# Kernel tuning notes

Measured on AMD Instinct MI355X. Metric: run time of the kernel, lower is better.

## Reference

```python
import jax, jax.numpy as jnp
import numpy as np

B, N, EMBED = 4, 2048, 512
H, EXPAND = 8, 3
D1 = (EXPAND * EMBED) // H * H   # 1536
HD = D1 // H                     # 192
RPE = int(min(EMBED / 8, 32))    # 32 (overridden in __init__)
EPS = 1e-8


def _srms(x, d):
    # SimpleRMSNorm: x / (||x||_2 * d^-0.5 + eps); no learnable params
    nrm = jnp.linalg.norm(x, axis=-1, keepdims=True)
    return x / (nrm * (d ** -0.5) + EPS)


def setup_inputs() -> dict:
    key = jax.random.key(0)
    ks = iter(jax.random.split(key, 32))
    w = lambda shape, s=0.02: jax.random.normal(next(ks), shape, dtype=jnp.float32) * s
    return {
        "xyz": jax.random.normal(next(ks), (B, N, 3), dtype=jnp.float32),
        "x": jax.random.normal(next(ks), (B, N, EMBED), dtype=jnp.float32),
        "u_w": w((EMBED, D1)), "u_b": w((D1,)),
        "v_w": w((EMBED, D1)), "v_b": w((D1,)),
        "o_w": w((D1, EMBED)), "o_b": w((EMBED,)),
        "rpe_pos_w": w((1, RPE)), "rpe_pos_b": w((RPE,)),
        "rpe_lyr_w": w((3, RPE, RPE)), "rpe_lyr_b": w((3, RPE)),
        "rpe_out_w": w((RPE, H * HD)), "rpe_out_b": w((H * HD,)),
        "glu1_w": w((EMBED, D1)), "glu1_b": w((D1,)),
        "glu2_w": w((EMBED, D1)), "glu2_b": w((D1,)),
        "glu3_w": w((D1, EMBED)), "glu3_b": w((EMBED,)),
    }


def _rpe_mlp(idx, pw, pb, lw, lb, ow, ob):
    # idx: [m, 1] positions -> [H, m, HD] Toeplitz coefficients
    h = jax.nn.relu(idx @ pw + pb)
    for i in range(lw.shape[0]):  # fixed small layer count (3), non-residual
        h = jax.nn.relu(_srms(h, RPE)) @ lw[i] + lb[i]
    o = jax.nn.relu(_srms(h, RPE)) @ ow + ob  # [m, H*HD]
    return o.reshape(-1, H, HD).transpose(1, 0, 2)


def reference(xyz, x, u_w, u_b, v_w, v_b, o_w, o_b,
              rpe_pos_w, rpe_pos_b, rpe_lyr_w, rpe_lyr_b,
              rpe_out_w, rpe_out_b,
              glu1_w, glu1_b, glu2_w, glu2_b, glu3_w, glu3_b):
    b, n, _ = x.shape
    shortcut = x
    # NOTE: original builds SimpleRMSNorm(d1) but applies it to embed_dim
    # features, so the divisor uses d1^-0.5. Preserved faithfully.
    xn = _srms(x, D1)
    u = jax.nn.silu(xn @ u_w + u_b)                      # b n d1
    v = jax.nn.silu(xn @ v_w + v_b)
    v = v.reshape(b, n, H, HD).transpose(0, 2, 1, 3)     # b h n d
    # --- Tno non-causal (par_type=1, no decay, act_type='none') ---
    rpe = lambda idx: _rpe_mlp(idx, rpe_pos_w, rpe_pos_b, rpe_lyr_w,
                               rpe_lyr_b, rpe_out_w, rpe_out_b)
    zero = rpe(jnp.zeros((1, 1), dtype=x.dtype))                     # h 1 d
    pos = rpe(jnp.arange(1, n, dtype=x.dtype)[:, None])              # h n-1 d
    neg = rpe(-jnp.arange(n - 1, 0, -1, dtype=x.dtype)[:, None])     # h n-1 d
    a = jnp.concatenate([zero, pos, zero, neg], axis=1)              # h 2n d
    # Toeplitz matmul as length-2n circular convolution via FFT
    yf = jnp.fft.rfft(v, 2 * n, axis=-2)
    af = jnp.fft.rfft(a, 2 * n, axis=-2)[None]
    t = jnp.fft.irfft(yf * af, 2 * n, axis=-2)[:, :, :n, :]          # b h n d
    t = t.transpose(0, 2, 1, 3).reshape(b, n, D1)
    out = (u * t) @ o_w + o_b
    x2 = out + shortcut
    # GLU (fina_act='None', dropout=0)
    g = (jax.nn.silu(x2 @ glu1_w + glu1_b) * (x2 @ glu2_w + glu2_b)) @ glu3_w + glu3_b
    return (g, out)
```

## Files before the change

kernel.cpp:

```cpp
#include <hip/hip_runtime.h>
#include <math.h>

#define NSEQ 2048
#define NFFT 4096
#define D1C  1536
#define EMBC 512
#define BATCH 4

typedef __fp16 f16;
typedef __fp16 f16x8 __attribute__((ext_vector_type(8)));
typedef __fp16 f16x4 __attribute__((ext_vector_type(4)));
typedef float  f32x4 __attribute__((ext_vector_type(4)));
typedef unsigned int u32;

__device__ __forceinline__ float silu_f(float y) { return y / (1.f + expf(-y)); }

__global__ __launch_bounds__(256) void scale_kernel(const float* __restrict__ x,
                                                    float* __restrict__ scale) {
    int row  = blockIdx.x * 4 + (threadIdx.x >> 6);
    int lane = threadIdx.x & 63;
    const float* xr = x + (size_t)row * EMBC;
    float ss = 0.f;
#pragma unroll
    for (int k = 0; k < EMBC / 64; ++k) { float v = xr[lane + k * 64]; ss += v * v; }
#pragma unroll
    for (int off = 32; off >= 1; off >>= 1) ss += __shfl_xor(ss, off);
    if (lane == 0) scale[row] = 1.f / (sqrtf(ss) * 0.02551551815399144f + 1e-8f);
}

__global__ __launch_bounds__(256) void convert_xn_kernel(
    const float* __restrict__ x, const float* __restrict__ scale,
    f16* __restrict__ xh, f16* __restrict__ xl) {
    size_t i = ((size_t)blockIdx.x * 256 + threadIdx.x) * 4;
    float4 v = *reinterpret_cast<const float4*>(x + i);
    float s = scale[i >> 9];
    f16x4 h, l;
    const float* vv = (const float*)&v;
#pragma unroll
    for (int j = 0; j < 4; ++j) {
        float val = vv[j] * s;
        f16 hh = (f16)val;
        h[j] = hh; l[j] = (f16)(val - (float)hh);
    }
    *reinterpret_cast<f16x4*>(xh + i) = h;
    *reinterpret_cast<f16x4*>(xl + i) = l;
}

__global__ __launch_bounds__(256) void convert_x2_kernel(
    const float* __restrict__ a, const float* __restrict__ b,
    f16* __restrict__ xh, f16* __restrict__ xl) {
    size_t i = ((size_t)blockIdx.x * 256 + threadIdx.x) * 4;
    float4 va = *reinterpret_cast<const float4*>(a + i);
    float4 vb = *reinterpret_cast<const float4*>(b + i);
    const float* pa = (const float*)&va;
    const float* pb = (const float*)&vb;
    f16x4 h, l;
#pragma unroll
    for (int j = 0; j < 4; ++j) {
        float val = pa[j] + pb[j];
        f16 hh = (f16)val;
        h[j] = hh; l[j] = (f16)(val - (float)hh);
    }
    *reinterpret_cast<f16x4*>(xh + i) = h;
    *reinterpret_cast<f16x4*>(xl + i) = l;
}

__global__ __launch_bounds__(256) void wtrans_kernel(const float* __restrict__ W,
        f16* __restrict__ Th, int Kd, int Nd) {
    __shared__ float t[32][33];
    int tx = threadIdx.x & 31, ty = threadIdx.x >> 5;
    int n0 = blockIdx.x * 32, k0 = blockIdx.y * 32;
#pragma unroll
    for (int yy = ty; yy < 32; yy += 8)
        t[yy][tx] = W[(size_t)(k0 + yy) * Nd + n0 + tx];
    __syncthreads();
#pragma unroll
    for (int yy = ty; yy < 32; yy += 8) {
        float v = t[tx][yy];
        Th[(size_t)(n0 + yy) * Kd + k0 + tx] = (f16)v;
    }
}

__global__ __launch_bounds__(256) void convert_p_kernel(
    const float* __restrict__ u, const float* __restrict__ vt,
    f16* __restrict__ ph, f16* __restrict__ pl) {
    __shared__ float t[32][33];
    int b = blockIdx.z, n0 = blockIdx.x * 32, c0 = blockIdx.y * 32;
    int tx = threadIdx.x & 31, ty = threadIdx.x >> 5;
#pragma unroll
    for (int yy = ty; yy < 32; yy += 8)
        t[yy][tx] = vt[(((size_t)(b * D1C + c0 + yy)) << 11) + n0 + tx];
    __syncthreads();
#pragma unroll
    for (int yy = ty; yy < 32; yy += 8) {
        int row = b * NSEQ + n0 + yy;
        size_t idx = (size_t)row * D1C + c0 + tx;
        float val = u[idx] * t[tx][yy];
        f16 h = (f16)val;
        ph[idx] = h; pl[idx] = (f16)(val - (float)h);
    }
}

__global__ __launch_bounds__(256) void rpe_kernel(
    const float* __restrict__ pw, const float* __restrict__ pb,
    const float* __restrict__ lw, const float* __restrict__ lb,
    const float* __restrict__ ow, const float* __restrict__ ob,
    float* __restrict__ a_r) {
    __shared__ float hs[64][33];
    int tid = threadIdx.x;
    int s0  = blockIdx.x * 64;
    if (tid < 64) {
        int s = s0 + tid;
        float p = (s == 0 || s == 2048) ? 0.f : (s < 2048 ? (float)s : (float)(s - 4096));
        float h[32];
#pragma unroll
        for (int k = 0; k < 32; ++k) h[k] = fmaxf(p * pw[k] + pb[k], 0.f);
        for (int L = 0; L < 3; ++L) {
            float ss = 0.f;
#pragma unroll
            for (int k = 0; k < 32; ++k) ss += h[k] * h[k];
            float sc = 1.f / (sqrtf(ss) * 0.1767766952966369f + 1e-8f);
            float g[32];
#pragma unroll
            for (int k = 0; k < 32; ++k) g[k] = fmaxf(h[k] * sc, 0.f);
#pragma unroll
            for (int j = 0; j < 32; ++j) {
                float acc = lb[L * 32 + j];
#pragma unroll
                for (int k = 0; k < 32; ++k) acc += g[k] * lw[(L * 32 + k) * 32 + j];
                h[j] = acc;
            }
        }
        float ss = 0.f;
#pragma unroll
        for (int k = 0; k < 32; ++k) ss += h[k] * h[k];
        float sc = 1.f / (sqrtf(ss) * 0.1767766952966369f + 1e-8f);
#pragma unroll
        for (int k = 0; k < 32; ++k) hs[tid][k] = fmaxf(h[k] * sc, 0.f);
    }
    __syncthreads();
    for (int cc = 0; cc < 6; ++cc) {
        int col = tid + cc * 256;
        float wcol[32];
#pragma unroll
        for (int k = 0; k < 32; ++k) wcol[k] = ow[k * D1C + col];
        float bb = ob[col];
        float* outp = a_r + ((size_t)col << 12) + s0;
        for (int r = 0; r < 64; ++r) {
            float acc = bb;
#pragma unroll
            for (int k = 0; k < 32; ++k) acc += hs[r][k] * wcol[k];
            outp[r] = acc;
        }
    }
}

#define LIDX(e) ((e) + ((((e) >> 4)) << 1))

template <bool INV, bool HALF>
__device__ __forceinline__ void dft16(const float* xr, const float* xi,
                                      float* outr, float* outi) {
    constexpr float C1 = 0.92387953251f, S1 = 0.38268343236f, R2 = 0.70710678119f;
    constexpr float sg = INV ? 1.f : -1.f;
    float tr[16], ti[16];
#pragma unroll
    for (int n0 = 0; n0 < 4; ++n0) {
        float ar = xr[n0], ai = xi[n0];
        float br = xr[n0 + 4], bi = xi[n0 + 4];
        float j0r, j0i, j1r, j1i, j2r, j2i, j3r, j3i;
        if constexpr (HALF) {
            j0r = ar + br; j0i = ai + bi;
            j2r = ar - br; j2i = ai - bi;
            if constexpr (!INV) { j1r = ar + bi; j1i = ai - br; j3r = ar - bi; j3i = ai + br; }
            else                { j1r = ar - bi; j1i = ai + br; j3r = ar + bi; j3i = ai - br; }
        } else {
            float cr = xr[n0 + 8],  ci = xi[n0 + 8];
            float dr = xr[n0 + 12], di = xi[n0 + 12];
            float t0r = ar + cr, t0i = ai + ci;
            float t1r = ar - cr, t1i = ai - ci;
            float t2r = br + dr, t2i = bi + di;
            float t3r = br - dr, t3i = bi - di;
            j0r = t0r + t2r; j0i = t0i + t2i;
            j2r = t0r - t2r; j2i = t0i - t2i;
            if constexpr (!INV) { j1r = t1r + t3i; j1i = t1i - t3r;
                                  j3r = t1r - t3i; j3i = t1i + t3r; }
            else                { j1r = t1r - t3i; j1i = t1i + t3r;
                                  j3r = t1r + t3i; j3i = t1i - t3r; }
        }
        tr[n0] = j0r;      ti[n0] = j0i;
        tr[n0 + 4] = j1r;  ti[n0 + 4] = j1i;
        tr[n0 + 8] = j2r;  ti[n0 + 8] = j2i;
        tr[n0 + 12] = j3r; ti[n0 + 12] = j3i;
    }
#define CMK(idx, wr_, wi_) { float _r = tr[idx], _i = ti[idx]; \
        tr[idx] = _r * (wr_) - _i * (wi_); ti[idx] = _r * (wi_) + _i * (wr_); }
    CMK(5,  C1, sg * S1)  CMK(6,  R2, sg * R2)  CMK(7,  S1, sg * C1)
    CMK(9,  R2, sg * R2)
    { float _r = tr[10];
      if constexpr (!INV) { tr[10] = ti[10];  ti[10] = -_r; }
      else                { tr[10] = -ti[10]; ti[10] = _r;  } }
    CMK(11, -R2, sg * R2)
    CMK(13, S1, sg * C1)  CMK(14, -R2, sg * R2)  CMK(15, -C1, -sg * S1)
#undef CMK
#pragma unroll
    for (int j = 0; j < 4; ++j) {
        float ar = tr[4 * j],     ai = ti[4 * j];
        float br = tr[4 * j + 1], bi = ti[4 * j + 1];
        float cr = tr[4 * j + 2], ci = ti[4 * j + 2];
        float dr = tr[4 * j + 3], di = ti[4 * j + 3];
        float t0r = ar + cr, t0i = ai + ci;
        float t1r = ar - cr, t1i = ai - ci;
        float t2r = br + dr, t2i = bi + di;
        float t3r = br - dr, t3i = bi - di;
        outr[j]      = t0r + t2r; outi[j]      = t0i + t2i;
        outr[8 + j]  = t0r - t2r; outi[8 + j]  = t0i - t2i;
        if constexpr (!INV) {
            outr[4 + j]  = t1r + t3i; outi[4 + j]  = t1i - t3r;
            outr[12 + j] = t1r - t3i; outi[12 + j] = t1i + t3r;
        } else {
            outr[4 + j]  = t1r - t3i; outi[4 + j]  = t1i + t3r;
            outr[12 + j] = t1r + t3i; outi[12 + j] = t1i - t3r;
        }
    }
}

#define CMUL_ADV(wr, wi, sr, si) { float _n = (wr)*(sr) - (wi)*(si); \
        (wi) = (wr)*(si) + (wi)*(sr); (wr) = _n; }

__global__ __launch_bounds__(256, 4) void fft_a_kernel(const float* __restrict__ a_r,
                                                       float2* __restrict__ af) {
    __shared__ float2 buf[4608];
    int tid = threadIdx.x;
    const float* row = a_r + ((size_t)blockIdx.x << 12);
    float2* orow     = af  + ((size_t)blockIdx.x << 12);
    float xr[16], xi[16], yr[16], yi[16];
    float bsr, bsi, wr, wi;
#pragma unroll
    for (int a = 0; a < 16; ++a) { xr[a] = row[a * 256 + tid]; xi[a] = 0.f; }
    dft16<false, false>(xr, xi, yr, yi);
    __sincosf(-(float)M_PI / 2048.f * (float)tid, &bsi, &bsr);
    wr = bsr; wi = bsi;
    buf[LIDX(tid)] = make_float2(yr[0], yi[0]);
#pragma unroll
    for (int k0 = 1; k0 < 16; ++k0) {
        buf[LIDX(k0 * 256 + tid)] =
            make_float2(yr[k0] * wr - yi[k0] * wi, yr[k0] * wi + yi[k0] * wr);
        CMUL_ADV(wr, wi, bsr, bsi);
    }
    __syncthreads();
    int k0 = tid >> 4, cc = tid & 15;
    int base2 = k0 * 256 + cc;
#pragma unroll
    for (int b = 0; b < 16; ++b) {
        float2 v = buf[LIDX(base2 + b * 16)]; xr[b] = v.x; xi[b] = v.y;
    }
    dft16<false, false>(xr, xi, yr, yi);
    __sincosf(-(float)M_PI / 128.f * (float)cc, &bsi, &bsr);
    wr = bsr; wi = bsi;
    buf[LIDX(base2)] = make_float2(yr[0], yi[0]);
#pragma unroll
    for (int k1 = 1; k1 < 16; ++k1) {
        buf[LIDX(base2 + k1 * 16)] =
            make_float2(yr[k1] * wr - yi[k1] * wi, yr[k1] * wi + yi[k1] * wr);
        CMUL_ADV(wr, wi, bsr, bsi);
    }
    __syncthreads();
    const float4* pld = (const float4*)&buf[18 * tid];
#pragma unroll
    for (int h = 0; h < 8; ++h) {
        float4 q = pld[h];
        xr[2 * h] = q.x; xi[2 * h] = q.y; xr[2 * h + 1] = q.z; xi[2 * h + 1] = q.w;
    }
    dft16<false, false>(xr, xi, yr, yi);
#pragma unroll
    for (int k2 = 0; k2 < 16; ++k2)
        orow[k2 * 256 + tid] = make_float2(yr[k2], yi[k2]);
}

__global__ __launch_bounds__(256, 4) void conv_kernel(float* __restrict__ vt,
                                                      const float2* __restrict__ af) {
    __shared__ float2 buf[4608];
    int tid = threadIdx.x;
    int pr  = blockIdx.x / D1C;
    int col = blockIdx.x % D1C;
    float* v0 = vt + ((size_t)((2 * pr)     * D1C + col) << 11);
    float* v1 = vt + ((size_t)((2 * pr + 1) * D1C + col) << 11);
    const float2* arow = af + ((size_t)col << 12);
    float xr[16], xi[16], yr[16], yi[16];
    float bsr, bsi, wr, wi;

#pragma unroll
    for (int a = 0; a < 8; ++a) { xr[a] = v0[a * 256 + tid]; xi[a] = v1[a * 256 + tid]; }
    dft16<false, true>(xr, xi, yr, yi);
    __sincosf(-(float)M_PI / 2048.f * (float)tid, &bsi, &bsr);
    wr = bsr; wi = bsi;
    buf[LIDX(tid)] = make_float2(yr[0], yi[0]);
#pragma unroll
    for (int k0 = 1; k0 < 16; ++k0) {
        buf[LIDX(k0 * 256 + tid)] =
            make_float2(yr[k0] * wr - yi[k0] * wi, yr[k0] * wi + yi[k0] * wr);
        CMUL_ADV(wr, wi, bsr, bsi);
    }
    __syncthreads();
    int k0 = tid >> 4, cc = tid & 15;
    int base2 = k0 * 256 + cc;
#pragma unroll
    for (int b = 0; b < 16; ++b) {
        float2 v = buf[LIDX(base2 + b * 16)]; xr[b] = v.x; xi[b] = v.y;
    }
    dft16<false, false>(xr, xi, yr, yi);
    __sincosf(-(float)M_PI / 128.f * (float)cc, &bsi, &bsr);
    wr = bsr; wi = bsi;
    buf[LIDX(base2)] = make_float2(yr[0], yi[0]);
#pragma unroll
    for (int k1 = 1; k1 < 16; ++k1) {
        buf[LIDX(base2 + k1 * 16)] =
            make_float2(yr[k1] * wr - yi[k1] * wi, yr[k1] * wi + yi[k1] * wr);
        CMUL_ADV(wr, wi, bsr, bsi);
    }
    __syncthreads();
    const float4* pld = (const float4*)&buf[18 * tid];
#pragma unroll
    for (int h = 0; h < 8; ++h) {
        float4 q = pld[h];
        xr[2 * h] = q.x; xi[2 * h] = q.y; xr[2 * h + 1] = q.z; xi[2 * h + 1] = q.w;
    }
    dft16<false, false>(xr, xi, yr, yi);
    const float inv = 1.0f / 4096.0f;
#pragma unroll
    for (int k2 = 0; k2 < 16; ++k2) {
        float2 w = arow[k2 * 256 + tid];
        float rr = (yr[k2] * w.x - yi[k2] * w.y) * inv;
        float ii = (yr[k2] * w.y + yi[k2] * w.x) * inv;
        xr[k2] = rr; xi[k2] = ii;
    }
    dft16<true, false>(xr, xi, yr, yi);
    __sincosf((float)M_PI / 128.f * (float)cc, &bsi, &bsr);
    wr = bsr; wi = bsi;
#pragma unroll
    for (int c = 1; c < 16; ++c) {
        float rr = yr[c] * wr - yi[c] * wi;
        yi[c] = yr[c] * wi + yi[c] * wr; yr[c] = rr;
        CMUL_ADV(wr, wi, bsr, bsi);
    }
    float4* pst = (float4*)&buf[18 * tid];
#pragma unroll
    for (int h = 0; h < 8; ++h)
        pst[h] = make_float4(yr[2 * h], yi[2 * h], yr[2 * h + 1], yi[2 * h + 1]);
    __syncthreads();
#pragma unroll
    for (int k1 = 0; k1 < 16; ++k1) {
        float2 v = buf[LIDX(base2 + k1 * 16)]; xr[k1] = v.x; xi[k1] = v.y;
    }
    dft16<true, false>(xr, xi, yr, yi);
    float swr, swi;
    __sincosf((float)M_PI / 2048.f * (float)(k0 * cc), &bsi, &bsr);
    __sincosf((float)M_PI / 128.f * (float)k0, &swi, &swr);
    wr = bsr; wi = bsi;
#pragma unroll
    for (int b = 0; b < 16; ++b) {
        buf[LIDX(base2 + b * 16)] =
            make_float2(yr[b] * wr - yi[b] * wi, yr[b] * wi + yi[b] * wr);
        CMUL_ADV(wr, wi, swr, swi);
    }
    __syncthreads();
#pragma unroll
    for (int k = 0; k < 16; ++k) {
        float2 v = buf[LIDX(k * 256 + tid)]; xr[k] = v.x; xi[k] = v.y;
    }
    dft16<true, false>(xr, xi, yr, yi);
#pragma unroll
    for (int a = 0; a < 8; ++a) {
        v0[a * 256 + tid] = yr[a];
        v1[a * 256 + tid] = yi[a];
    }
}

enum { EP_SILU_F32, EP_SILU_VT, EP_PLAIN, EP_GLU2 };

template <int BM, int K, int EPI>
__global__ __launch_bounds__(256, (BM == 128 ? 3 : 4)) void mgemm(
    const f16* __restrict__ Ah, const f16* __restrict__ Al,
    const f16* __restrict__ Bh,
    const float* __restrict__ bias, const float* __restrict__ E0,
    float* __restrict__ OutF, f16* __restrict__ OutH, f16* __restrict__ OutL,
    int Ncols) {
    constexpr int SB   = BM * 128 + 8192;
    constexpr int MREP = BM / 32;
    constexpr int LOGB = (BM == 128 ? 7 : 6);
    constexpr int CA   = BM / 64;
    __shared__ __align__(16) char smem[2 * SB];

    const int tid  = threadIdx.x;
    const int w    = tid >> 6, lane = tid & 63;
    const int wr   = w >> 1, wc = w & 1;
    const int l15  = lane & 15, kc = lane >> 4;

    const int NBY = Ncols >> 7;
    const int nwg = gridDim.x;
    int flat = blockIdx.x;
    int q8 = nwg >> 3, r8 = nwg & 7;
    int xcd = flat & 7, pos = flat >> 3;
    int wg = (xcd < r8 ? xcd * (q8 + 1) : r8 * (q8 + 1) + (xcd - r8) * q8) + pos;
    const int row0 = (wg / NBY) * BM;
    const int col0 = (wg % NBY) * 128;

    f32x4 acc[MREP][4] = {};

    auto stage = [&](int buf, int kt) {
        const int k0 = kt * 32;
        const int bb = buf * SB;
#pragma unroll
        for (int l = 0; l < CA; ++l) {
            int ci = tid + l * 256;
            int r = ci & (BM - 1), kk = ci >> LOGB;
            const f16* ga = Ah + (size_t)(row0 + r) * K + k0 + kk * 8;
            const f16* gb = Al + (size_t)(row0 + r) * K + k0 + kk * 8;
            __builtin_amdgcn_global_load_lds((const __attribute__((address_space(1))) u32*)ga,
                (__attribute__((address_space(3))) u32*)(smem + bb + ci * 16), 16, 0, 0);
            __builtin_amdgcn_global_load_lds((const __attribute__((address_space(1))) u32*)gb,
                (__attribute__((address_space(3))) u32*)(smem + bb + BM * 64 + ci * 16), 16, 0, 0);
        }
#pragma unroll
        for (int l = 0; l < 2; ++l) {
            int ci = tid + l * 256;
            int c = ci & 127, kk = ci >> 7;
            const f16* gc = Bh + (size_t)(col0 + c) * K + k0 + kk * 8;
            __builtin_amdgcn_global_load_lds((const __attribute__((address_space(1))) u32*)gc,
                (__attribute__((address_space(3))) u32*)(smem + bb + BM * 128 + ci * 16), 16, 0, 0);
        }
    };

    auto compute = [&](int buf) {
        const char* base = smem + buf * SB;
        f16x8 a_h[MREP], a_l[MREP], b_h[4];
#pragma unroll
        for (int m = 0; m < MREP; ++m) {
            int r = wr * (BM / 2) + m * 16 + l15;
            a_h[m] = *(const f16x8*)(base + (kc * BM + r) * 16);
            a_l[m] = *(const f16x8*)(base + BM * 64 + (kc * BM + r) * 16);
        }
#pragma unroll
        for (int n = 0; n < 4; ++n) {
            int c = wc * 64 + n * 16 + l15;
            b_h[n] = *(const f16x8*)(base + BM * 128 + (kc * 128 + c) * 16);
        }
#pragma unroll
        for (int m = 0; m < MREP; ++m)
#pragma unroll
            for (int n = 0; n < 4; ++n) {
                acc[m][n] = __builtin_amdgcn_mfma_f32_16x16x32_f16(a_h[m], b_h[n], acc[m][n], 0, 0, 0);
                acc[m][n] = __builtin_amdgcn_mfma_f32_16x16x32_f16(a_l[m], b_h[n], acc[m][n], 0, 0, 0);
            }
    };

    constexpr int NT = K / 32;
    stage(0, 0);
    __syncthreads();
    int cur = 0;
    for (int t = 0; t < NT; ++t) {
        if (t + 1 < NT) stage(cur ^ 1, t + 1);
        compute(cur);
        __syncthreads();
        cur ^= 1;
    }

    const int WRB = wr * (BM / 2);
    if constexpr (EPI == EP_SILU_VT) {
        float* patch = (float*)(smem + w * 5376);
#pragma unroll
        for (int m = 0; m < MREP; ++m) {
            __syncthreads();
#pragma unroll
            for (int n = 0; n < 4; ++n)
#pragma unroll
                for (int r = 0; r < 4; ++r)
                    patch[(n * 16 + l15) * 20 + kc * 4 + r] = acc[m][n][r];
            __syncthreads();
#pragma unroll
            for (int t = 0; t < 4; ++t) {
                int qi = lane + t * 64;
                int col_ = qi >> 2, rq = qi & 3;
                float4 y = *(const float4*)&patch[col_ * 20 + rq * 4];
                int col = col0 + wc * 64 + col_;
                float bb = bias[col];
                y.x = silu_f(y.x + bb); y.y = silu_f(y.y + bb);
                y.z = silu_f(y.z + bb); y.w = silu_f(y.w + bb);
                int b = row0 >> 11;
                int seq = (row0 & 2047) + WRB + m * 16 + rq * 4;
                *(float4*)&OutF[(((size_t)(b * D1C + col)) << 11) + seq] = y;
            }
        }
    } else {
        float* patch = (float*)(smem + w * 4352);
#pragma unroll
        for (int m = 0; m < MREP; ++m) {
            __syncthreads();
#pragma unroll
            for (int n = 0; n < 4; ++n)
#pragma unroll
                for (int r = 0; r < 4; ++r)
                    patch[(kc * 4 + r) * 68 + n * 16 + l15] = acc[m][n][r];
            __syncthreads();
#pragma unroll
            for (int t = 0; t < 4; ++t) {
                int qi = lane + t * 64;
                int row_ = qi >> 4, q = qi & 15;
                float4 y = *(const float4*)&patch[row_ * 68 + q * 4];
                int row = row0 + WRB + m * 16 + row_;
                int col = col0 + wc * 64 + q * 4;
                float4 bb = *(const float4*)&bias[col];
                y.x += bb.x; y.y += bb.y; y.z += bb.z; y.w += bb.w;
                size_t idx = (size_t)row * Ncols + col;
                if constexpr (EPI == EP_SILU_F32) {
                    y.x = silu_f(y.x); y.y = silu_f(y.y);
                    y.z = silu_f(y.z); y.w = silu_f(y.w);
                    *(float4*)&OutF[idx] = y;
                } else if constexpr (EPI == EP_PLAIN) {
                    *(float4*)&OutF[idx] = y;
                } else {
                    float4 e = *(const float4*)&E0[idx];
                    float z0 = e.x * y.x, z1 = e.y * y.y, z2 = e.z * y.z, z3 = e.w * y.w;
                    f16x4 h, l;
                    h[0] = (f16)z0; l[0] = (f16)(z0 - (float)h[0]);
                    h[1] = (f16)z1; l[1] = (f16)(z1 - (float)h[1]);
                    h[2] = (f16)z2; l[2] = (f16)(z2 - (float)h[2]);
                    h[3] = (f16)z3; l[3] = (f16)(z3 - (float)h[3]);
                    *(f16x4*)&OutH[idx] = h;
                    *(f16x4*)&OutL[idx] = l;
                }
            }
        }
    }
}

extern "C" void kernel_launch(void* const* d_in, const int* in_sizes, int n_in,
                              void* d_out, int out_size, void* d_ws, size_t ws_size,
                              hipStream_t stream) {
    const float* x   = (const float*)d_in[1];
    const float* u_w = (const float*)d_in[2];
    const float* u_b = (const float*)d_in[3];
    const float* v_w = (const float*)d_in[4];
    const float* v_b = (const float*)d_in[5];
    const float* o_w = (const float*)d_in[6];
    const float* o_b = (const float*)d_in[7];
    const float* rpw = (const float*)d_in[8];
    const float* rpb = (const float*)d_in[9];
    const float* rlw = (const float*)d_in[10];
    const float* rlb = (const float*)d_in[11];
    const float* row_w = (const float*)d_in[12];
    const float* rob = (const float*)d_in[13];
    const float* g1w = (const float*)d_in[14];
    const float* g1b = (const float*)d_in[15];
    const float* g2w = (const float*)d_in[16];
    const float* g2b = (const float*)d_in[17];
    const float* g3w = (const float*)d_in[18];
    const float* g3b = (const float*)d_in[19];

    char* wsb = (char*)d_ws;
    float* scale = (float*)wsb;
    char* R1 = wsb + (1 << 16);
    char* R2 = R1 + 50331648;
    char* R3 = R2 + 50331648;
    char* R4 = R3 + 50331648;
    char* R5 = R4 + 16777216;

    float2* af   = (float2*)R1;
    f16*    ph   = (f16*)R1;
    f16*    pl   = (f16*)(R1 + 25165824);
    float*  vt   = (float*)R2;
    float*  tmp1 = (float*)R2;
    float*  a_r  = (float*)R3;
    float*  u    = (float*)R3;
    f16*    zh   = (f16*)R3;
    f16*    zl   = (f16*)(R3 + 25165824);
    f16*    xnh  = (f16*)R4;
    f16*    xnl  = (f16*)(R4 + 8388608);
    f16*    x2h  = xnh;
    f16*    x2l  = xnl;

    auto wTh = [&](int i) { return (f16*)(R5 + (size_t)i * 1572864); };

    float* g_out   = (float*)d_out;
    float* out_out = g_out + (size_t)BATCH * NSEQ * EMBC;

    scale_kernel<<<2048, 256, 0, stream>>>(x, scale);
    convert_xn_kernel<<<4096, 256, 0, stream>>>(x, scale, xnh, xnl);
    wtrans_kernel<<<dim3(48, 16), 256, 0, stream>>>(u_w, wTh(0), 512, 1536);
    wtrans_kernel<<<dim3(48, 16), 256, 0, stream>>>(v_w, wTh(1), 512, 1536);
    wtrans_kernel<<<dim3(16, 48), 256, 0, stream>>>(o_w, wTh(2), 1536, 512);
    wtrans_kernel<<<dim3(48, 16), 256, 0, stream>>>(g1w, wTh(3), 512, 1536);
    wtrans_kernel<<<dim3(48, 16), 256, 0, stream>>>(g2w, wTh(4), 512, 1536);
    wtrans_kernel<<<dim3(16, 48), 256, 0, stream>>>(g3w, wTh(5), 1536, 512);
    rpe_kernel<<<64, 256, 0, stream>>>(rpw, rpb, rlw, rlb, row_w, rob, a_r);
    fft_a_kernel<<<1536, 256, 0, stream>>>(a_r, af);

    mgemm<128, 512, EP_SILU_F32><<<768, 256, 0, stream>>>(
        xnh, xnl, wTh(0), u_b, nullptr, u, nullptr, nullptr, 1536);
    mgemm<128, 512, EP_SILU_VT><<<768, 256, 0, stream>>>(
        xnh, xnl, wTh(1), v_b, nullptr, vt, nullptr, nullptr, 1536);

    conv_kernel<<<3072, 256, 0, stream>>>(vt, af);
    convert_p_kernel<<<dim3(64, 48, 4), 256, 0, stream>>>(u, vt, ph, pl);

    mgemm<64, 1536, EP_PLAIN><<<512, 256, 0, stream>>>(
        ph, pl, wTh(2), o_b, nullptr, out_out, nullptr, nullptr, 512);

    convert_x2_kernel<<<4096, 256, 0, stream>>>(out_out, x, x2h, x2l);
    mgemm<128, 512, EP_SILU_F32><<<768, 256, 0, stream>>>(
        x2h, x2l, wTh(3), g1b, nullptr, tmp1, nullptr, nullptr, 1536);
    mgemm<128, 512, EP_GLU2><<<768, 256, 0, stream>>>(
        x2h, x2l, wTh(4), g2b, tmp1, nullptr, zh, zl, 1536);
    mgemm<64, 1536, EP_PLAIN><<<512, 256, 0, stream>>>(
        zh, zl, wTh(5), g3b, nullptr, g_out, nullptr, nullptr, 512);
}
```

Baseline: 676.0 us.

## Fuse RPE output projection into FFT kernel, store only hidden activations

The RPE MLP kernel now writes only the 32-wide normalized hidden activations, transposed, with one thread per position across all 256-thread blocks. Each FFT block recomputes its column of the output projection (32 FMAs per element) directly into registers before the forward DFT. This removes the 1536x4096 float intermediate write and read and the poorly parallel 64-block projection loop, at the cost of redundant hidden-activation reads per column. The DFT helper now works in place to cut register arrays, and the FFT kernels' occupancy hint drops from 4 to 3 blocks per multiprocessor.

```diff
diff --git a/kernel.cpp b/kernel.cpp
--- a/kernel.cpp
+++ b/kernel.cpp
@@ -101,65 +101,43 @@
     }
 }
 
-__global__ __launch_bounds__(256) void rpe_kernel(
+__global__ __launch_bounds__(256) void rpe_mlp_kernel(
     const float* __restrict__ pw, const float* __restrict__ pb,
     const float* __restrict__ lw, const float* __restrict__ lb,
-    const float* __restrict__ ow, const float* __restrict__ ob,
-    float* __restrict__ a_r) {
-    __shared__ float hs[64][33];
-    int tid = threadIdx.x;
-    int s0  = blockIdx.x * 64;
-    if (tid < 64) {
-        int s = s0 + tid;
-        float p = (s == 0 || s == 2048) ? 0.f : (s < 2048 ? (float)s : (float)(s - 4096));
-        float h[32];
-#pragma unroll
-        for (int k = 0; k < 32; ++k) h[k] = fmaxf(p * pw[k] + pb[k], 0.f);
-        for (int L = 0; L < 3; ++L) {
-            float ss = 0.f;
-#pragma unroll
-            for (int k = 0; k < 32; ++k) ss += h[k] * h[k];
-            float sc = 1.f / (sqrtf(ss) * 0.1767766952966369f + 1e-8f);
-            float g[32];
-#pragma unroll
-            for (int k = 0; k < 32; ++k) g[k] = fmaxf(h[k] * sc, 0.f);
-#pragma unroll
-            for (int j = 0; j < 32; ++j) {
-                float acc = lb[L * 32 + j];
-#pragma unroll
-                for (int k = 0; k < 32; ++k) acc += g[k] * lw[(L * 32 + k) * 32 + j];
-                h[j] = acc;
-            }
-        }
+    float* __restrict__ hgT) {
+    int s = blockIdx.x * 256 + threadIdx.x;
+    float p = (s == 0 || s == 2048) ? 0.f : (s < 2048 ? (float)s : (float)(s - 4096));
+    float h[32];
+#pragma unroll
+    for (int k = 0; k < 32; ++k) h[k] = fmaxf(p * pw[k] + pb[k], 0.f);
+    for (int L = 0; L < 3; ++L) {
         float ss = 0.f;
 #pragma unroll
         for (int k = 0; k < 32; ++k) ss += h[k] * h[k];
         float sc = 1.f / (sqrtf(ss) * 0.1767766952966369f + 1e-8f);
-#pragma unroll
-        for (int k = 0; k < 32; ++k) hs[tid][k] = fmaxf(h[k] * sc, 0.f);
-    }
-    __syncthreads();
-    for (int cc = 0; cc < 6; ++cc) {
-        int col = tid + cc * 256;
-        float wcol[32];
-#pragma unroll
-        for (int k = 0; k < 32; ++k) wcol[k] = ow[k * D1C + col];
-        float bb = ob[col];
-        float* outp = a_r + ((size_t)col << 12) + s0;
-        for (int r = 0; r < 64; ++r) {
-            float acc = bb;
-#pragma unroll
-            for (int k = 0; k < 32; ++k) acc += hs[r][k] * wcol[k];
-            outp[r] = acc;
-        }
-    }
+        float g[32];
+#pragma unroll
+        for (int k = 0; k < 32; ++k) g[k] = fmaxf(h[k] * sc, 0.f);
+#pragma unroll
+        for (int j = 0; j < 32; ++j) {
+            float acc = lb[L * 32 + j];
+#pragma unroll
+            for (int k = 0; k < 32; ++k) acc += g[k] * lw[(L * 32 + k) * 32 + j];
+            h[j] = acc;
+        }
+    }
+    float ss = 0.f;
+#pragma unroll
+    for (int k = 0; k < 32; ++k) ss += h[k] * h[k];
+    float sc = 1.f / (sqrtf(ss) * 0.1767766952966369f + 1e-8f);
+#pragma unroll
+    for (int k = 0; k < 32; ++k) hgT[(k << 12) + s] = fmaxf(h[k] * sc, 0.f);
 }
 
 #define LIDX(e) ((e) + ((((e) >> 4)) << 1))
 
 template <bool INV, bool HALF>
-__device__ __forceinline__ void dft16(const float* xr, const float* xi,
-                                      float* outr, float* outi) {
+__device__ __forceinline__ void dft16(float* xr, float* xi) {
     constexpr float C1 = 0.92387953251f, S1 = 0.38268343236f, R2 = 0.70710678119f;
     constexpr float sg = INV ? 1.f : -1.f;
     float tr[16], ti[16];
@@ -212,14 +190,14 @@
         float t1r = ar - cr, t1i = ai - ci;
         float t2r = br + dr, t2i = bi + di;
         float t3r = br - dr, t3i = bi - di;
-        outr[j]      = t0r + t2r; outi[j]      = t0i + t2i;
-        outr[8 + j]  = t0r - t2r; outi[8 + j]  = t0i - t2i;
+        xr[j]      = t0r + t2r; xi[j]      = t0i + t2i;
+        xr[8 + j]  = t0r - t2r; xi[8 + j]  = t0i - t2i;
         if constexpr (!INV) {
-            outr[4 + j]  = t1r + t3i; outi[4 + j]  = t1i - t3r;
-            outr[12 + j] = t1r - t3i; outi[12 + j] = t1i + t3r;
+            xr[4 + j]  = t1r + t3i; xi[4 + j]  = t1i - t3r;
+            xr[12 + j] = t1r - t3i; xi[12 + j] = t1i + t3r;
         } else {
-            outr[4 + j]  = t1r - t3i; outi[4 + j]  = t1i + t3r;
-            outr[12 + j] = t1r + t3i; outi[12 + j] = t1i - t3r;
+            xr[4 + j]  = t1r - t3i; xi[4 + j]  = t1i + t3r;
+            xr[12 + j] = t1r + t3i; xi[12 + j] = t1i - t3r;
         }
     }
 }
@@ -227,24 +205,32 @@
 #define CMUL_ADV(wr, wi, sr, si) { float _n = (wr)*(sr) - (wi)*(si); \
         (wi) = (wr)*(si) + (wi)*(sr); (wr) = _n; }
 
-__global__ __launch_bounds__(256, 4) void fft_a_kernel(const float* __restrict__ a_r,
-                                                       float2* __restrict__ af) {
+__global__ __launch_bounds__(256, 3) void fft_a_kernel(
+    const float* __restrict__ hgT, const float* __restrict__ ow,
+    const float* __restrict__ ob, float2* __restrict__ af) {
     __shared__ float2 buf[4608];
     int tid = threadIdx.x;
-    const float* row = a_r + ((size_t)blockIdx.x << 12);
-    float2* orow     = af  + ((size_t)blockIdx.x << 12);
-    float xr[16], xi[16], yr[16], yi[16];
+    int col = blockIdx.x;
+    float2* orow = af + ((size_t)col << 12);
+    float xr[16], xi[16];
     float bsr, bsi, wr, wi;
-#pragma unroll
-    for (int a = 0; a < 16; ++a) { xr[a] = row[a * 256 + tid]; xi[a] = 0.f; }
-    dft16<false, false>(xr, xi, yr, yi);
+    float obc = ob[col];
+#pragma unroll
+    for (int a = 0; a < 16; ++a) { xr[a] = obc; xi[a] = 0.f; }
+    for (int k = 0; k < 32; ++k) {
+        float wk = ow[k * D1C + col];
+        const float* hrow = hgT + (k << 12) + tid;
+#pragma unroll
+        for (int a = 0; a < 16; ++a) xr[a] = fmaf(hrow[a * 256], wk, xr[a]);
+    }
+    dft16<false, false>(xr, xi);
     __sincosf(-(float)M_PI / 2048.f * (float)tid, &bsi, &bsr);
     wr = bsr; wi = bsi;
-    buf[LIDX(tid)] = make_float2(yr[0], yi[0]);
+    buf[LIDX(tid)] = make_float2(xr[0], xi[0]);
 #pragma unroll
     for (int k0 = 1; k0 < 16; ++k0) {
         buf[LIDX(k0 * 256 + tid)] =
-            make_float2(yr[k0] * wr - yi[k0] * wi, yr[k0] * wi + yi[k0] * wr);
+            make_float2(xr[k0] * wr - xi[k0] * wi, xr[k0] * wi + xi[k0] * wr);
         CMUL_ADV(wr, wi, bsr, bsi);
     }
     __syncthreads();
@@ -254,14 +240,14 @@
     for (int b = 0; b < 16; ++b) {
         float2 v = buf[LIDX(base2 + b * 16)]; xr[b] = v.x; xi[b] = v.y;
     }
-    dft16<false, false>(xr, xi, yr, yi);
+    dft16<false, false>(xr, xi);
     __sincosf(-(float)M_PI / 128.f * (float)cc, &bsi, &bsr);
     wr = bsr; wi = bsi;
-    buf[LIDX(base2)] = make_float2(yr[0], yi[0]);
+    buf[LIDX(base2)] = make_float2(xr[0], xi[0]);
 #pragma unroll
     for (int k1 = 1; k1 < 16; ++k1) {
         buf[LIDX(base2 + k1 * 16)] =
-            make_float2(yr[k1] * wr - yi[k1] * wi, yr[k1] * wi + yi[k1] * wr);
+            make_float2(xr[k1] * wr - xi[k1] * wi, xr[k1] * wi + xi[k1] * wr);
         CMUL_ADV(wr, wi, bsr, bsi);
     }
     __syncthreads();
@@ -271,13 +257,13 @@
         float4 q = pld[h];
         xr[2 * h] = q.x; xi[2 * h] = q.y; xr[2 * h + 1] = q.z; xi[2 * h + 1] = q.w;
     }
-    dft16<false, false>(xr, xi, yr, yi);
+    dft16<false, false>(xr, xi);
 #pragma unroll
     for (int k2 = 0; k2 < 16; ++k2)
-        orow[k2 * 256 + tid] = make_float2(yr[k2], yi[k2]);
-}
-
-__global__ __launch_bounds__(256, 4) void conv_kernel(float* __restrict__ vt,
+        orow[k2 * 256 + tid] = make_float2(xr[k2], xi[k2]);
+}
+
+__global__ __launch_bounds__(256, 3) void conv_kernel(float* __restrict__ vt,
                                                       const float2* __restrict__ af) {
     __shared__ float2 buf[4608];
     int tid = threadIdx.x;
@@ -286,19 +272,19 @@
     float* v0 = vt + ((size_t)((2 * pr)     * D1C + col) << 11);
     float* v1 = vt + ((size_t)((2 * pr + 1) * D1C + col) << 11);
     const float2* arow = af + ((size_t)col << 12);
-    float xr[16], xi[16], yr[16], yi[16];
+    float xr[16], xi[16];
     float bsr, bsi, wr, wi;
 
 #pragma unroll
     for (int a = 0; a < 8; ++a) { xr[a] = v0[a * 256 + tid]; xi[a] = v1[a * 256 + tid]; }
-    dft16<false, true>(xr, xi, yr, yi);
+    dft16<false, true>(xr, xi);
     __sincosf(-(float)M_PI / 2048.f * (float)tid, &bsi, &bsr);
     wr = bsr; wi = bsi;
-    buf[LIDX(tid)] = make_float2(yr[0], yi[0]);
+    buf[LIDX(tid)] = make_float2(xr[0], xi[0]);
 #pragma unroll
     for (int k0 = 1; k0 < 16; ++k0) {
         buf[LIDX(k0 * 256 + tid)] =
-            make_float2(yr[k0] * wr - yi[k0] * wi, yr[k0] * wi + yi[k0] * wr);
+            make_float2(xr[k0] * wr - xi[k0] * wi, xr[k0] * wi + xi[k0] * wr);
         CMUL_ADV(wr, wi, bsr, bsi);
     }
     __syncthreads();
@@ -308,14 +294,14 @@
     for (int b = 0; b < 16; ++b) {
         float2 v = buf[LIDX(base2 + b * 16)]; xr[b] = v.x; xi[b] = v.y;
     }
-    dft16<false, false>(xr, xi, yr, yi);
+    dft16<false, false>(xr, xi);
     __sincosf(-(float)M_PI / 128.f * (float)cc, &bsi, &bsr);
     wr = bsr; wi = bsi;
-    buf[LIDX(base2)] = make_float2(yr[0], yi[0]);
+    buf[LIDX(base2)] = make_float2(xr[0], xi[0]);
 #pragma unroll
     for (int k1 = 1; k1 < 16; ++k1) {
         buf[LIDX(base2 + k1 * 16)] =
-            make_float2(yr[k1] * wr - yi[k1] * wi, yr[k1] * wi + yi[k1] * wr);
+            make_float2(xr[k1] * wr - xi[k1] * wi, xr[k1] * wi + xi[k1] * wr);
         CMUL_ADV(wr, wi, bsr, bsi);
     }
     __syncthreads();
@@ -325,34 +311,34 @@
         float4 q = pld[h];
         xr[2 * h] = q.x; xi[2 * h] = q.y; xr[2 * h + 1] = q.z; xi[2 * h + 1] = q.w;
     }
-    dft16<false, false>(xr, xi, yr, yi);
+    dft16<false, false>(xr, xi);
     const float inv = 1.0f / 4096.0f;
 #pragma unroll
     for (int k2 = 0; k2 < 16; ++k2) {
         float2 w = arow[k2 * 256 + tid];
-        float rr = (yr[k2] * w.x - yi[k2] * w.y) * inv;
-        float ii = (yr[k2] * w.y + yi[k2] * w.x) * inv;
+        float rr = (xr[k2] * w.x - xi[k2] * w.y) * inv;
+        float ii = (xr[k2] * w.y + xi[k2] * w.x) * inv;
         xr[k2] = rr; xi[k2] = ii;
     }
-    dft16<true, false>(xr, xi, yr, yi);
+    dft16<true, false>(xr, xi);
     __sincosf((float)M_PI / 128.f * (float)cc, &bsi, &bsr);
     wr = bsr; wi = bsi;
 #pragma unroll
     for (int c = 1; c < 16; ++c) {
-        float rr = yr[c] * wr - yi[c] * wi;
-        yi[c] = yr[c] * wi + yi[c] * wr; yr[c] = rr;
+        float rr = xr[c] * wr - xi[c] * wi;
+        xi[c] = xr[c] * wi + xi[c] * wr; xr[c] = rr;
         CMUL_ADV(wr, wi, bsr, bsi);
     }
     float4* pst = (float4*)&buf[18 * tid];
 #pragma unroll
     for (int h = 0; h < 8; ++h)
-        pst[h] = make_float4(yr[2 * h], yi[2 * h], yr[2 * h + 1], yi[2 * h + 1]);
+        pst[h] = make_float4(xr[2 * h], xi[2 * h], xr[2 * h + 1], xi[2 * h + 1]);
     __syncthreads();
 #pragma unroll
     for (int k1 = 0; k1 < 16; ++k1) {
         float2 v = buf[LIDX(base2 + k1 * 16)]; xr[k1] = v.x; xi[k1] = v.y;
     }
-    dft16<true, false>(xr, xi, yr, yi);
+    dft16<true, false>(xr, xi);
     float swr, swi;
     __sincosf((float)M_PI / 2048.f * (float)(k0 * cc), &bsi, &bsr);
     __sincosf((float)M_PI / 128.f * (float)k0, &swi, &swr);
@@ -360,7 +346,7 @@
 #pragma unroll
     for (int b = 0; b < 16; ++b) {
         buf[LIDX(base2 + b * 16)] =
-            make_float2(yr[b] * wr - yi[b] * wi, yr[b] * wi + yi[b] * wr);
+            make_float2(xr[b] * wr - xi[b] * wi, xr[b] * wi + xi[b] * wr);
         CMUL_ADV(wr, wi, swr, swi);
     }
     __syncthreads();
@@ -368,11 +354,11 @@
     for (int k = 0; k < 16; ++k) {
         float2 v = buf[LIDX(k * 256 + tid)]; xr[k] = v.x; xi[k] = v.y;
     }
-    dft16<true, false>(xr, xi, yr, yi);
+    dft16<true, false>(xr, xi);
 #pragma unroll
     for (int a = 0; a < 8; ++a) {
-        v0[a * 256 + tid] = yr[a];
-        v1[a * 256 + tid] = yi[a];
+        v0[a * 256 + tid] = xr[a];
+        v1[a * 256 + tid] = xi[a];
     }
 }
 
@@ -570,7 +556,7 @@
     f16*    pl   = (f16*)(R1 + 25165824);
     float*  vt   = (float*)R2;
     float*  tmp1 = (float*)R2;
-    float*  a_r  = (float*)R3;
+    float*  hgT  = (float*)R3;
     float*  u    = (float*)R3;
     f16*    zh   = (f16*)R3;
     f16*    zl   = (f16*)(R3 + 25165824);
@@ -592,8 +578,8 @@
     wtrans_kernel<<<dim3(48, 16), 256, 0, stream>>>(g1w, wTh(3), 512, 1536);
     wtrans_kernel<<<dim3(48, 16), 256, 0, stream>>>(g2w, wTh(4), 512, 1536);
     wtrans_kernel<<<dim3(16, 48), 256, 0, stream>>>(g3w, wTh(5), 1536, 512);
-    rpe_kernel<<<64, 256, 0, stream>>>(rpw, rpb, rlw, rlb, row_w, rob, a_r);
-    fft_a_kernel<<<1536, 256, 0, stream>>>(a_r, af);
+    rpe_mlp_kernel<<<16, 256, 0, stream>>>(rpw, rpb, rlw, rlb, hgT);
+    fft_a_kernel<<<1536, 256, 0, stream>>>(hgT, row_w, rob, af);
 
     mgemm<128, 512, EP_SILU_F32><<<768, 256, 0, stream>>>(
         xnh, xnl, wTh(0), u_b, nullptr, u, nullptr, nullptr, 1536);
```

Measured after the change: 584.2 us. 13.6% less time.
